# Kernel optimization log

Measured on AMD Instinct MI355X. Metric: run time of the kernel, lower is better.

The kernel has to match this reference:

```python
import jax, jax.numpy as jnp
import numpy as np

B, INS, OUTS, REF, H, NH, DH, NL, DFF = 8, 32, 64, 8, 256, 8, 32, 6, 1024
N = OUTS * OUTS  # 4096 tokens


def _ln(x, g, b, eps=1e-5):
    m = x.mean(-1, keepdims=True)
    v = ((x - m) ** 2).mean(-1, keepdims=True)
    return (x - m) * jax.lax.rsqrt(v + eps) * g + b


def _resize_ac(x, out):
    Hin = x.shape[1]
    c = jnp.arange(out) * ((Hin - 1) / (out - 1))
    i0 = jnp.floor(c).astype(jnp.int32)
    i1 = jnp.minimum(i0 + 1, Hin - 1)
    w = (c - i0).astype(x.dtype)
    x = x[:, i0] * (1 - w)[None, :, None, None] + x[:, i1] * w[None, :, None, None]
    x = x[:, :, i0] * (1 - w)[None, None, :, None] + x[:, :, i1] * w[None, None, :, None]
    return x


def _pos_embedding():
    # unified_pos_embedding: distance from each 64x64 grid point to each 8x8 ref point -> [N, REF^2]
    g = jnp.linspace(0.0, 1.0, OUTS)
    gx, gy = jnp.meshgrid(g, g, indexing='ij')
    grid = jnp.stack([gx, gy], -1).reshape(N, 2)
    r = jnp.linspace(0.0, 1.0, REF)
    rx, ry = jnp.meshgrid(r, r, indexing='ij')
    rgrid = jnp.stack([rx, ry], -1).reshape(REF * REF, 2)
    return jnp.sqrt(((grid[:, None, :] - rgrid[None, :, :]) ** 2).sum(-1))


def setup_inputs() -> dict:
    key = jax.random.key(0)
    ks = iter(jax.random.split(key, 64))
    def nrm(shape, std=0.02):
        return jax.random.normal(next(ks), shape, jnp.float32) * std
    inp = {'x': jax.random.normal(next(ks), (B, INS, INS, 3), jnp.float32)}
    inp['pre_W1'] = nrm((1 + REF * REF, 2 * H)); inp['pre_b1'] = jnp.zeros((2 * H,))
    inp['pre_W2'] = nrm((2 * H, H)); inp['pre_b2'] = jnp.zeros((H,))
    inp['placeholder'] = jax.random.uniform(next(ks), (H,), jnp.float32) / H
    inp['ln1_g'] = jnp.ones((NL, H)); inp['ln1_b'] = jnp.zeros((NL, H))
    inp['ln1a_g'] = jnp.ones((NL, H)); inp['ln1a_b'] = jnp.zeros((NL, H))
    inp['Wq'] = nrm((NL, H, H)); inp['Wk'] = nrm((NL, H, H)); inp['Wv'] = nrm((NL, H, H))
    inp['Wo'] = nrm((NL, H, H)); inp['bo'] = jnp.zeros((NL, H))
    inp['kn_g'] = jnp.ones((NL, NH, DH)); inp['kn_b'] = jnp.zeros((NL, NH, DH))
    inp['vn_g'] = jnp.ones((NL, NH, DH)); inp['vn_b'] = jnp.zeros((NL, NH, DH))
    inp['ln2_g'] = jnp.ones((NL, H)); inp['ln2_b'] = jnp.zeros((NL, H))
    inp['mlp_W1'] = nrm((NL, H, DFF)); inp['mlp_b1'] = jnp.zeros((NL, DFF))
    inp['mlp_W2'] = nrm((NL, DFF, H)); inp['mlp_b2'] = jnp.zeros((NL, H))
    inp['ln3_g'] = jnp.ones((H,)); inp['ln3_b'] = jnp.zeros((H,))
    inp['out_W'] = nrm((H, 1)); inp['out_b'] = jnp.zeros((1,))
    return inp


def reference(x, pre_W1, pre_b1, pre_W2, pre_b2, placeholder,
              ln1_g, ln1_b, ln1a_g, ln1a_b, Wq, Wk, Wv, Wo, bo,
              kn_g, kn_b, vn_g, vn_b, ln2_g, ln2_b,
              mlp_W1, mlp_b1, mlp_W2, mlp_b2, ln3_g, ln3_b, out_W, out_b):
    Bsz = x.shape[0]
    xr = _resize_ac(x, OUTS)[..., 2:3]          # [B,64,64,1]
    fx = xr.reshape(Bsz, N, 1)
    pos = _pos_embedding()                       # [N,64]
    fx = jnp.concatenate([fx, jnp.broadcast_to(pos[None], (Bsz, N, REF * REF))], -1)
    h = jax.nn.gelu(fx @ pre_W1 + pre_b1, approximate=False) @ pre_W2 + pre_b2
    h = h + placeholder
    for i in range(NL):
        xq = _ln(h, ln1_g[i], ln1_b[i])
        xkv = _ln(h, ln1a_g[i], ln1a_b[i])
        q = (xq @ Wq[i]).reshape(Bsz, N, NH, DH).transpose(0, 2, 1, 3)
        k = (xkv @ Wk[i]).reshape(Bsz, N, NH, DH).transpose(0, 2, 1, 3)
        v = (xkv @ Wv[i]).reshape(Bsz, N, NH, DH).transpose(0, 2, 1, 3)
        # galerkin attention: layernorm K and V over head dim (per-head affine), no softmax
        k = _ln(k, kn_g[i][:, None, :], kn_b[i][:, None, :])
        v = _ln(v, vn_g[i][:, None, :], vn_b[i][:, None, :])
        ctx = jnp.einsum('bhnd,bhne->bhde', k, v) / N   # [B,h,d,d]
        att = jnp.einsum('bhnd,bhde->bhne', q, ctx)
        att = att.transpose(0, 2, 1, 3).reshape(Bsz, N, H) @ Wo[i] + bo[i]
        h = h + att
        y = _ln(h, ln2_g[i], ln2_b[i])
        h = h + (jax.nn.gelu(y @ mlp_W1[i] + mlp_b1[i], approximate=False) @ mlp_W2[i] + mlp_b2[i])
    out = _ln(h, ln3_g, ln3_b) @ out_W + out_b
    return out.reshape(Bsz, OUTS, OUTS, 1)
```

## Files before the change

kernel.cpp:

```cpp
#include <hip/hip_runtime.h>
#include <cmath>

#define B_    8
#define INS_  32
#define OUTS_ 64
#define REF_  8
#define H_    256
#define NH_   8
#define DH_   32
#define NL_   6
#define DFF_  1024
#define N_    4096
#define M_    (B_*N_)
#define BUF   8388608ull

typedef unsigned short u16;
typedef unsigned int   u32;
typedef __attribute__((ext_vector_type(8))) short  bf16x8;
typedef __attribute__((ext_vector_type(4))) float  f32x4;
typedef __attribute__((ext_vector_type(4))) unsigned short u16x4;

struct bfpair { u16 hi, lo; };

__device__ __forceinline__ float gelu_f(float x){
    return 0.5f * x * (1.0f + erff(x * 0.70710678118654752f));
}
__device__ __forceinline__ u16 f2b(float f){
    union { float f; u32 u; } v; v.f = f;
    u32 r = v.u + 0x7fffu + ((v.u >> 16) & 1u);
    return (u16)(r >> 16);
}
__device__ __forceinline__ float b2f(u16 b){
    union { u32 u; float f; } v; v.u = ((u32)b) << 16;
    return v.f;
}
__device__ __forceinline__ bfpair fsplit(float x){
    bfpair p;
    p.hi = f2b(x);
    p.lo = f2b(x - b2f(p.hi));
    return p;
}

__global__ __launch_bounds__(256) void tconv_kernel(const float* __restrict__ in,
                                                    u16* __restrict__ oh,
                                                    u16* __restrict__ ol,
                                                    int K, int N, int Kpad, int nl,
                                                    int lstride)
{
    int idx = blockIdx.x * 256 + threadIdx.x;
    int per = N * Kpad;
    if (idx >= nl * per) return;
    int l = idx / per;
    int rem = idx - l * per;
    int n = rem / Kpad;
    int k = rem - n * Kpad;
    float v = (k < K) ? in[(size_t)l * K * N + (size_t)k * N + n] : 0.0f;
    bfpair p = fsplit(v);
    size_t o = (size_t)l * lstride + (size_t)n * Kpad + k;
    oh[o] = p.hi; ol[o] = p.lo;
}

__global__ __launch_bounds__(256) void lnfold_kernel(const float* __restrict__ kg,
                                                     const float* __restrict__ kb,
                                                     const float* __restrict__ vg,
                                                     const float* __restrict__ vb,
                                                     float* __restrict__ lng,
                                                     float* __restrict__ lnb)
{
    int idx = blockIdx.x * 256 + threadIdx.x;
    if (idx >= NL_ * 512) return;
    int l = idx >> 9, c = idx & 511;
    if (c < 256) { lng[idx] = kg[l * 256 + c];       lnb[idx] = kb[l * 256 + c]; }
    else         { lng[idx] = vg[l * 256 + c - 256]; lnb[idx] = vb[l * 256 + c - 256]; }
}

__global__ __launch_bounds__(256) void fx_kernel(const float* __restrict__ x,
                                                 u16* __restrict__ fh,
                                                 u16* __restrict__ fl)
{
    int idx = blockIdx.x * 256 + threadIdx.x;
    const int total = M_ * 96;
    if (idx >= total) return;
    int f   = idx % 96;
    int row = idx / 96;
    int n   = row % N_;
    int b   = row / N_;
    int gi = n >> 6, gj = n & 63;
    float v = 0.0f;
    if (f == 0) {
        float ci = gi * (31.0f / 63.0f);
        float cj = gj * (31.0f / 63.0f);
        int i0 = (int)floorf(ci); int i1 = min(i0 + 1, 31);
        int j0 = (int)floorf(cj); int j1 = min(j0 + 1, 31);
        float wi = ci - (float)i0, wj = cj - (float)j0;
        const float* xb = x + (size_t)b * INS_ * INS_ * 3 + 2;
        float v00 = xb[(i0 * 32 + j0) * 3];
        float v01 = xb[(i0 * 32 + j1) * 3];
        float v10 = xb[(i1 * 32 + j0) * 3];
        float v11 = xb[(i1 * 32 + j1) * 3];
        float r0 = v00 * (1.0f - wi) + v10 * wi;
        float r1 = v01 * (1.0f - wi) + v11 * wi;
        v = r0 * (1.0f - wj) + r1 * wj;
    } else if (f < 65) {
        int r = f - 1;
        int ri = r >> 3, rj = r & 7;
        float dx = gi * (1.0f / 63.0f) - ri * (1.0f / 7.0f);
        float dy = gj * (1.0f / 63.0f) - rj * (1.0f / 7.0f);
        v = sqrtf(dx * dx + dy * dy);
    }
    bfpair p = fsplit(v);
    fh[idx] = p.hi; fl[idx] = p.lo;
}

template<int EPI, int BN, int TERMS>
__global__ __launch_bounds__(256) void gemm_split(const u16* __restrict__ Ah,
                                                  const u16* __restrict__ Al,
                                                  const u16* __restrict__ Bh,
                                                  const u16* __restrict__ Bl,
                                                  float* __restrict__ Cf,
                                                  u16* __restrict__ Ch,
                                                  u16* __restrict__ Cl,
                                                  const float* __restrict__ bias,
                                                  const float* __restrict__ bias2,
                                                  const float* __restrict__ lng,
                                                  const float* __restrict__ lnb,
                                                  int M, int Nn, int K, int bstride)
{
    constexpr int NREP = BN / 32;
    constexpr int BROUNDS = BN / 64;
    __shared__ u16 AsH[4096];
    __shared__ u16 BsH[BN * 32];
    __shared__ u16 AsL[TERMS >= 2 ? 4096 : 1];
    __shared__ u16 BsL[TERMS == 3 ? BN * 32 : 1];
    const int tid = threadIdx.x;
    const int nwgx = gridDim.x;
    const int nwg  = nwgx * gridDim.y;
    const int bid  = blockIdx.y * nwgx + blockIdx.x;
    const int swz  = (bid & 7) * (nwg >> 3) + (bid >> 3);
    const int bm = (swz / nwgx) * 128;
    const int bn = (swz % nwgx) * BN;
    const u16* BhB = Bh + (size_t)(bm >> 12) * bstride;
    const u16* BlB = Bl + (size_t)(bm >> 12) * bstride;
    const int l  = tid & 63;
    const int w  = tid >> 6;
    const int wr = w >> 1, wc = w & 1;
    const int lrow = l & 15;
    const int kh   = l >> 4;

    f32x4 acc[4][NREP];
    #pragma unroll
    for (int m = 0; m < 4; ++m)
        #pragma unroll
        for (int n = 0; n < NREP; ++n)
            acc[m][n] = (f32x4){0.0f, 0.0f, 0.0f, 0.0f};

    for (int k0 = 0; k0 < K; k0 += 32) {
        #pragma unroll
        for (int i = 0; i < 2; ++i) {
            int L = i * 256 + tid;
            int row = L >> 2, ch = L & 3;
            size_t goffA = (size_t)(bm + row) * K + k0 + ch * 8;
            __builtin_amdgcn_global_load_lds(
                (const __attribute__((address_space(1))) void*)(Ah + goffA),
                (__attribute__((address_space(3))) void*)(AsH + L * 8), 16, 0, 0);
            if constexpr (TERMS >= 2)
                __builtin_amdgcn_global_load_lds(
                    (const __attribute__((address_space(1))) void*)(Al + goffA),
                    (__attribute__((address_space(3))) void*)(AsL + L * 8), 16, 0, 0);
        }
        #pragma unroll
        for (int i = 0; i < BROUNDS; ++i) {
            int L = i * 256 + tid;
            int row = L >> 2, ch = L & 3;
            size_t goffB = (size_t)(bn + row) * K + k0 + ch * 8;
            __builtin_amdgcn_global_load_lds(
                (const __attribute__((address_space(1))) void*)(BhB + goffB),
                (__attribute__((address_space(3))) void*)(BsH + L * 8), 16, 0, 0);
            if constexpr (TERMS == 3)
                __builtin_amdgcn_global_load_lds(
                    (const __attribute__((address_space(1))) void*)(BlB + goffB),
                    (__attribute__((address_space(3))) void*)(BsL + L * 8), 16, 0, 0);
        }
        __syncthreads();
        bf16x8 afh[4], afl[4], bfh[NREP], bfl[NREP];
        #pragma unroll
        for (int m = 0; m < 4; ++m) {
            int off = (wr * 64 + m * 16 + lrow) * 32 + kh * 8;
            afh[m] = *(const bf16x8*)(AsH + off);
            if constexpr (TERMS >= 2) afl[m] = *(const bf16x8*)(AsL + off);
        }
        #pragma unroll
        for (int n = 0; n < NREP; ++n) {
            int off = (wc * (BN / 2) + n * 16 + lrow) * 32 + kh * 8;
            bfh[n] = *(const bf16x8*)(BsH + off);
            if constexpr (TERMS == 3) bfl[n] = *(const bf16x8*)(BsL + off);
        }
        #pragma unroll
        for (int m = 0; m < 4; ++m)
            #pragma unroll
            for (int n = 0; n < NREP; ++n) {
                acc[m][n] = __builtin_amdgcn_mfma_f32_16x16x32_bf16(afh[m], bfh[n], acc[m][n], 0, 0, 0);
                if constexpr (TERMS >= 2)
                    acc[m][n] = __builtin_amdgcn_mfma_f32_16x16x32_bf16(afl[m], bfh[n], acc[m][n], 0, 0, 0);
                if constexpr (TERMS == 3)
                    acc[m][n] = __builtin_amdgcn_mfma_f32_16x16x32_bf16(afh[m], bfl[n], acc[m][n], 0, 0, 0);
            }
        __syncthreads();
    }

    const int row0 = bm + wr * 64;
    const int col0 = bn + wc * (BN / 2);

    if constexpr (EPI == 4) {
        #pragma unroll
        for (int m = 0; m < 4; ++m) {
            #pragma unroll
            for (int j = 0; j < 4; ++j) {
                int r = row0 + m * 16 + kh * 4 + j;
                #pragma unroll
                for (int hp = 0; hp < NREP / 2; ++hp) {
                    float a0 = acc[m][2 * hp + 0][j];
                    float a1 = acc[m][2 * hp + 1][j];
                    float s = a0 + a1;
                    s += __shfl_xor(s, 1); s += __shfl_xor(s, 2);
                    s += __shfl_xor(s, 4); s += __shfl_xor(s, 8);
                    float mean = s * (1.0f / 32.0f);
                    float d0 = a0 - mean, d1 = a1 - mean;
                    float q = d0 * d0 + d1 * d1;
                    q += __shfl_xor(q, 1); q += __shfl_xor(q, 2);
                    q += __shfl_xor(q, 4); q += __shfl_xor(q, 8);
                    float rstd = rsqrtf(q * (1.0f / 32.0f) + 1e-5f);
                    #pragma unroll
                    for (int t = 0; t < 2; ++t) {
                        int n = 2 * hp + t;
                        int col = col0 + n * 16 + lrow;
                        float dd = t ? d1 : d0;
                        float o = dd * rstd * lng[col] + lnb[col];
                        bfpair p = fsplit(o);
                        size_t idx = (size_t)r * Nn + col;
                        Ch[idx] = p.hi; Cl[idx] = p.lo;
                    }
                }
            }
        }
        return;
    }

    #pragma unroll
    for (int m = 0; m < 4; ++m) {
        #pragma unroll
        for (int n = 0; n < NREP; ++n) {
            int col = col0 + n * 16 + lrow;
            float bv = bias ? bias[col] : 0.0f;
            if (EPI == 3) bv += bias2[col];
            #pragma unroll
            for (int j = 0; j < 4; ++j) {
                int r = row0 + m * 16 + kh * 4 + j;
                float v = acc[m][n][j] + bv;
                size_t idx = (size_t)r * Nn + col;
                if (EPI == 0) {
                    bfpair p = fsplit(v);
                    Ch[idx] = p.hi; Cl[idx] = p.lo;
                } else if (EPI == 1) {
                    bfpair p = fsplit(gelu_f(v));
                    Ch[idx] = p.hi; Cl[idx] = p.lo;
                } else if (EPI == 2) {
                    Cf[idx] += v;
                } else {
                    Cf[idx] = v;
                }
            }
        }
    }
}

__global__ __launch_bounds__(256) void ln_dual_kernel(const float* __restrict__ h,
                                                      u16* __restrict__ o1h,
                                                      u16* __restrict__ o1l,
                                                      u16* __restrict__ o2h,
                                                      u16* __restrict__ o2l,
                                                      const float* __restrict__ g1,
                                                      const float* __restrict__ b1,
                                                      const float* __restrict__ g2,
                                                      const float* __restrict__ b2)
{
    int row  = blockIdx.x * 4 + (threadIdx.x >> 6);
    int lane = threadIdx.x & 63;
    const float4 v = ((const float4*)(h + (size_t)row * H_))[lane];
    float s = v.x + v.y + v.z + v.w;
    #pragma unroll
    for (int m = 1; m < 64; m <<= 1) s += __shfl_xor(s, m, 64);
    float mean = s * (1.0f / H_);
    float dx = v.x - mean, dy = v.y - mean, dz = v.z - mean, dw = v.w - mean;
    float sq = dx * dx + dy * dy + dz * dz + dw * dw;
    #pragma unroll
    for (int m = 1; m < 64; m <<= 1) sq += __shfl_xor(sq, m, 64);
    float rstd = rsqrtf(sq * (1.0f / H_) + 1e-5f);

    float4 G = ((const float4*)g1)[lane];
    float4 Bv = ((const float4*)b1)[lane];
    u16x4 oh, ol;
    bfpair p0 = fsplit(dx * rstd * G.x + Bv.x);
    bfpair p1 = fsplit(dy * rstd * G.y + Bv.y);
    bfpair p2 = fsplit(dz * rstd * G.z + Bv.z);
    bfpair p3 = fsplit(dw * rstd * G.w + Bv.w);
    oh.x = p0.hi; ol.x = p0.lo;
    oh.y = p1.hi; ol.y = p1.lo;
    oh.z = p2.hi; ol.z = p2.lo;
    oh.w = p3.hi; ol.w = p3.lo;
    ((u16x4*)(o1h + (size_t)row * H_))[lane] = oh;
    ((u16x4*)(o1l + (size_t)row * H_))[lane] = ol;
    if (o2h) {
        G = ((const float4*)g2)[lane];
        Bv = ((const float4*)b2)[lane];
        p0 = fsplit(dx * rstd * G.x + Bv.x);
        p1 = fsplit(dy * rstd * G.y + Bv.y);
        p2 = fsplit(dz * rstd * G.z + Bv.z);
        p3 = fsplit(dw * rstd * G.w + Bv.w);
        oh.x = p0.hi; ol.x = p0.lo;
        oh.y = p1.hi; ol.y = p1.lo;
        oh.z = p2.hi; ol.z = p2.lo;
        oh.w = p3.hi; ol.w = p3.lo;
        ((u16x4*)(o2h + (size_t)row * H_))[lane] = oh;
        ((u16x4*)(o2l + (size_t)row * H_))[lane] = ol;
    }
}

__global__ __launch_bounds__(256) void ctx_partial_kernel(const u16* __restrict__ kvh,
                                                          const u16* __restrict__ kvl,
                                                          float* __restrict__ ctxp)
{
    int bh = blockIdx.x;
    int split = blockIdx.y;
    int b = bh >> 3, hd = bh & 7;
    __shared__ float kc[8][32], vc[8][32];
    int tid = threadIdx.x;
    int rd = tid >> 5, dd = tid & 31;
    int d  = tid >> 3;
    int e0 = (tid & 7) * 4;
    float a0 = 0, a1 = 0, a2 = 0, a3 = 0;
    int nbase = split * 512;
    for (int it = 0; it < 64; ++it) {
        size_t off = ((size_t)(b * N_ + nbase + it * 8 + rd)) * 512 + hd * 32 + dd;
        kc[rd][dd] = b2f(kvh[off]) + b2f(kvl[off]);
        vc[rd][dd] = b2f(kvh[off + 256]) + b2f(kvl[off + 256]);
        __syncthreads();
        #pragma unroll
        for (int r = 0; r < 8; ++r) {
            float kd = kc[r][d];
            a0 += kd * vc[r][e0 + 0];
            a1 += kd * vc[r][e0 + 1];
            a2 += kd * vc[r][e0 + 2];
            a3 += kd * vc[r][e0 + 3];
        }
        __syncthreads();
    }
    float* out = ctxp + ((size_t)(split * 64 + bh)) * 1024 + d * 32 + e0;
    out[0] = a0; out[1] = a1; out[2] = a2; out[3] = a3;
}

__global__ __launch_bounds__(256) void compose1_kernel(const float* __restrict__ ctxp,
                                                       const float* __restrict__ Wo,
                                                       float* __restrict__ G)
{
    int b  = blockIdx.x >> 3;
    int hd = blockIdx.x & 7;
    __shared__ float cl[32][32];
    __shared__ float wl[32][256];
    int tid = threadIdx.x;
    {
        const float* src = ctxp + ((size_t)(b * 8 + hd)) * 1024;
        #pragma unroll
        for (int i = 0; i < 4; ++i) {
            float s = 0.0f;
            #pragma unroll
            for (int sp = 0; sp < 8; ++sp)
                s += src[(size_t)sp * 65536 + tid + 256 * i];
            ((float*)cl)[tid + 256 * i] = s * (1.0f / N_);
        }
        #pragma unroll
        for (int i = 0; i < 32; ++i)
            wl[i][tid] = Wo[(size_t)(hd * 32 + i) * 256 + tid];
    }
    __syncthreads();
    int j = tid;
    for (int d = 0; d < 32; ++d) {
        float s = 0.0f;
        #pragma unroll
        for (int e = 0; e < 32; ++e) s += cl[d][e] * wl[e][j];
        G[((size_t)b * 256 + hd * 32 + d) * 256 + j] = s;
    }
}

__global__ __launch_bounds__(256) void compose2_kernel(const float* __restrict__ Wq,
                                                       const float* __restrict__ G,
                                                       u16* __restrict__ fh,
                                                       u16* __restrict__ fl)
{
    int b  = blockIdx.x;
    int jg = blockIdx.y;
    __shared__ float Gs[16][256];
    int tid = threadIdx.x;
    #pragma unroll
    for (int jj = 0; jj < 16; ++jj)
        Gs[jj][tid] = G[(size_t)b * 65536 + (size_t)tid * 256 + jg * 16 + jj];
    __syncthreads();
    int i = tid;
    float acc[16];
    #pragma unroll
    for (int jj = 0; jj < 16; ++jj) acc[jj] = 0.0f;
    for (int m = 0; m < 256; ++m) {
        float wv = Wq[(size_t)i * 256 + m];
        #pragma unroll
        for (int jj = 0; jj < 16; ++jj) acc[jj] += wv * Gs[jj][m];
    }
    #pragma unroll
    for (int jj = 0; jj < 16; ++jj) {
        bfpair p = fsplit(acc[jj]);
        size_t off = (size_t)b * 65536 + (size_t)(jg * 16 + jj) * 256 + i;
        fh[off] = p.hi; fl[off] = p.lo;
    }
}

__global__ __launch_bounds__(256) void final_kernel(const float* __restrict__ h,
                                                    const float* __restrict__ g,
                                                    const float* __restrict__ bb,
                                                    const float* __restrict__ W,
                                                    const float* __restrict__ ob,
                                                    float* __restrict__ out)
{
    int row  = blockIdx.x * 4 + (threadIdx.x >> 6);
    int lane = threadIdx.x & 63;
    const float4 v = ((const float4*)(h + (size_t)row * H_))[lane];
    float s = v.x + v.y + v.z + v.w;
    #pragma unroll
    for (int m = 1; m < 64; m <<= 1) s += __shfl_xor(s, m, 64);
    float mean = s * (1.0f / H_);
    float dx = v.x - mean, dy = v.y - mean, dz = v.z - mean, dw = v.w - mean;
    float sq = dx * dx + dy * dy + dz * dz + dw * dw;
    #pragma unroll
    for (int m = 1; m < 64; m <<= 1) sq += __shfl_xor(sq, m, 64);
    float rstd = rsqrtf(sq * (1.0f / H_) + 1e-5f);
    float4 G = ((const float4*)g)[lane];
    float4 Bv = ((const float4*)bb)[lane];
    float4 Wv = ((const float4*)W)[lane];
    float s2 = (dx * rstd * G.x + Bv.x) * Wv.x
             + (dy * rstd * G.y + Bv.y) * Wv.y
             + (dz * rstd * G.z + Bv.z) * Wv.z
             + (dw * rstd * G.w + Bv.w) * Wv.w;
    #pragma unroll
    for (int m = 1; m < 64; m <<= 1) s2 += __shfl_xor(s2, m, 64);
    if (lane == 0) out[row] = s2 + ob[0];
}

extern "C" void kernel_launch(void* const* d_in, const int* in_sizes, int n_in,
                              void* d_out, int out_size, void* d_ws, size_t ws_size,
                              hipStream_t stream)
{
    const float* x        = (const float*)d_in[0];
    const float* pre_W1   = (const float*)d_in[1];
    const float* pre_b1   = (const float*)d_in[2];
    const float* pre_W2   = (const float*)d_in[3];
    const float* pre_b2   = (const float*)d_in[4];
    const float* placeholder = (const float*)d_in[5];
    const float* ln1_g    = (const float*)d_in[6];
    const float* ln1_b    = (const float*)d_in[7];
    const float* ln1a_g   = (const float*)d_in[8];
    const float* ln1a_b   = (const float*)d_in[9];
    const float* Wq       = (const float*)d_in[10];
    const float* Wk       = (const float*)d_in[11];
    const float* Wv       = (const float*)d_in[12];
    const float* Wo       = (const float*)d_in[13];
    const float* bo       = (const float*)d_in[14];
    const float* kn_g     = (const float*)d_in[15];
    const float* kn_b     = (const float*)d_in[16];
    const float* vn_g     = (const float*)d_in[17];
    const float* vn_b     = (const float*)d_in[18];
    const float* ln2_g    = (const float*)d_in[19];
    const float* ln2_b    = (const float*)d_in[20];
    const float* mlp_W1   = (const float*)d_in[21];
    const float* mlp_b1   = (const float*)d_in[22];
    const float* mlp_W2   = (const float*)d_in[23];
    const float* mlp_b2   = (const float*)d_in[24];
    const float* ln3_g    = (const float*)d_in[25];
    const float* ln3_b    = (const float*)d_in[26];
    const float* out_W    = (const float*)d_in[27];
    const float* out_b    = (const float*)d_in[28];

    float* ws   = (float*)d_ws;
    float* h    = ws;
    float* ctxp = ws + BUF;
    float* Gbuf = ctxp + 524288;
    float* lng  = Gbuf + 524288;
    float* lnb  = lng + NL_ * 512;
    u16* ub = (u16*)(lnb + NL_ * 512);
    u16* xa_h = ub;
    u16* xa_l = xa_h + BUF;
    u16* xb_h = xa_l + BUF;
    u16* xb_l = xb_h + BUF;
    u16* kv_h = xb_l + BUF;
    u16* kv_l = kv_h + 2 * BUF;
    u16* wt   = kv_l + 2 * BUF;
    u16* w_pre1h = wt;               u16* w_pre1l = w_pre1h + 49152;
    u16* w_pre2h = w_pre1l + 49152;  u16* w_pre2l = w_pre2h + 131072;
    u16* w_kvh = w_pre2l + 131072;   u16* w_kvl = w_kvh + 786432;
    u16* w_m1h = w_kvl + 786432;     u16* w_m1l = w_m1h + 1572864;
    u16* w_m2h = w_m1l + 1572864;    u16* w_m2l = w_m2h + 1572864;
    u16* f_h   = w_m2l + 1572864;    u16* f_l   = f_h + 524288;

    tconv_kernel<<<(512 * 96 + 255) / 256, 256, 0, stream>>>(pre_W1, w_pre1h, w_pre1l, 65, 512, 96, 1, 49152);
    tconv_kernel<<<(256 * 512 + 255) / 256, 256, 0, stream>>>(pre_W2, w_pre2h, w_pre2l, 512, 256, 512, 1, 131072);
    tconv_kernel<<<(6 * 65536 + 255) / 256, 256, 0, stream>>>(Wk, w_kvh, w_kvl, 256, 256, 256, 6, 131072);
    tconv_kernel<<<(6 * 65536 + 255) / 256, 256, 0, stream>>>(Wv, w_kvh + 65536, w_kvl + 65536, 256, 256, 256, 6, 131072);
    tconv_kernel<<<(6 * 262144 + 255) / 256, 256, 0, stream>>>(mlp_W1, w_m1h, w_m1l, 256, 1024, 256, 6, 262144);
    tconv_kernel<<<(6 * 262144 + 255) / 256, 256, 0, stream>>>(mlp_W2, w_m2h, w_m2l, 1024, 256, 1024, 6, 262144);
    lnfold_kernel<<<(NL_ * 512 + 255) / 256, 256, 0, stream>>>(kn_g, kn_b, vn_g, vn_b, lng, lnb);

    fx_kernel<<<(M_ * 96 + 255) / 256, 256, 0, stream>>>(x, xa_h, xa_l);
    for (int half = 0; half < 2; ++half) {
        size_t ao = (size_t)half * (M_ / 2) * 96;
        gemm_split<1, 128, 3><<<dim3(512 / 128, (M_ / 2) / 128), 256, 0, stream>>>(
            xa_h + ao, xa_l + ao, w_pre1h, w_pre1l, nullptr, xb_h, xb_l,
            pre_b1, nullptr, nullptr, nullptr, M_ / 2, 512, 96, 0);
        gemm_split<3, 128, 3><<<dim3(256 / 128, (M_ / 2) / 128), 256, 0, stream>>>(
            xb_h, xb_l, w_pre2h, w_pre2l, h + (size_t)half * (M_ / 2) * H_,
            nullptr, nullptr, pre_b2, placeholder, nullptr, nullptr, M_ / 2, 256, 512, 0);
    }

    for (int l = 0; l < NL_; ++l) {
        ln_dual_kernel<<<M_ / 4, 256, 0, stream>>>(
            h, xa_h, xa_l, xb_h, xb_l, ln1_g + l * H_, ln1_b + l * H_,
            ln1a_g + l * H_, ln1a_b + l * H_);

        gemm_split<4, 128, 2><<<dim3(512 / 128, M_ / 128), 256, 0, stream>>>(
            xb_h, xb_l, w_kvh + (size_t)l * 131072, w_kvl + (size_t)l * 131072,
            nullptr, kv_h, kv_l, nullptr, nullptr,
            lng + l * 512, lnb + l * 512, M_, 512, H_, 0);

        ctx_partial_kernel<<<dim3(64, 8), 256, 0, stream>>>(kv_h, kv_l, ctxp);
        compose1_kernel<<<64, 256, 0, stream>>>(ctxp, Wo + (size_t)l * 65536, Gbuf);
        compose2_kernel<<<dim3(8, 16), 256, 0, stream>>>(Wq + (size_t)l * 65536, Gbuf, f_h, f_l);

        gemm_split<2, 64, 2><<<dim3(256 / 64, M_ / 128), 256, 0, stream>>>(
            xa_h, xa_l, f_h, f_l, h, nullptr, nullptr, bo + l * H_, nullptr,
            nullptr, nullptr, M_, H_, H_, 65536);

        ln_dual_kernel<<<M_ / 4, 256, 0, stream>>>(
            h, xa_h, xa_l, nullptr, nullptr, ln2_g + l * H_, ln2_b + l * H_, nullptr, nullptr);

        for (int half = 0; half < 2; ++half) {
            size_t ao = (size_t)half * (M_ / 2) * H_;
            gemm_split<1, 128, 3><<<dim3(DFF_ / 128, (M_ / 2) / 128), 256, 0, stream>>>(
                xa_h + ao, xa_l + ao, w_m1h + (size_t)l * 262144, w_m1l + (size_t)l * 262144,
                nullptr, xb_h, kv_h, mlp_b1 + (size_t)l * DFF_, nullptr,
                nullptr, nullptr, M_ / 2, DFF_, H_, 0);
            gemm_split<2, 64, 3><<<dim3(256 / 64, (M_ / 2) / 128), 256, 0, stream>>>(
                xb_h, kv_h, w_m2h + (size_t)l * 262144, w_m2l + (size_t)l * 262144,
                h + ao, nullptr, nullptr, mlp_b2 + (size_t)l * H_, nullptr,
                nullptr, nullptr, M_ / 2, H_, DFF_, 0);
        }
    }

    final_kernel<<<M_ / 4, 256, 0, stream>>>(
        h, ln3_g, ln3_b, out_W, out_b, (float*)d_out);
}
```

Before: 2.179 ms.

## Double-buffer LDS tiles in split GEMM and merge pre-MLP halves

The split-bf16 GEMM now uses two LDS buffers per operand and issues the global-to-LDS loads for the next K tile before computing on the current one, so load latency can overlap the MFMA work. The pre-embedding MLP no longer runs in two halves; both GEMMs cover all rows in one launch each, with the larger kv buffers holding the 512-wide intermediate. This doubles LDS use per block, which can lower occupancy, especially for the 3-term variant. The loop still syncs only once per iteration, so correctness depends on the next-stage loads not being visible to the MFMA reads before the barrier.

```diff
diff --git a/kernel.cpp b/kernel.cpp
--- a/kernel.cpp
+++ b/kernel.cpp
@@ -128,10 +128,10 @@
 {
     constexpr int NREP = BN / 32;
     constexpr int BROUNDS = BN / 64;
-    __shared__ u16 AsH[4096];
-    __shared__ u16 BsH[BN * 32];
-    __shared__ u16 AsL[TERMS >= 2 ? 4096 : 1];
-    __shared__ u16 BsL[TERMS == 3 ? BN * 32 : 1];
+    __shared__ u16 AsH[2][4096];
+    __shared__ u16 BsH[2][BN * 32];
+    __shared__ u16 AsL[TERMS >= 2 ? 2 : 1][TERMS >= 2 ? 4096 : 1];
+    __shared__ u16 BsL[TERMS == 3 ? 2 : 1][TERMS == 3 ? BN * 32 : 1];
     const int tid = threadIdx.x;
     const int nwgx = gridDim.x;
     const int nwg  = nwgx * gridDim.y;
@@ -147,14 +147,7 @@
     const int lrow = l & 15;
     const int kh   = l >> 4;
 
-    f32x4 acc[4][NREP];
-    #pragma unroll
-    for (int m = 0; m < 4; ++m)
-        #pragma unroll
-        for (int n = 0; n < NREP; ++n)
-            acc[m][n] = (f32x4){0.0f, 0.0f, 0.0f, 0.0f};
-
-    for (int k0 = 0; k0 < K; k0 += 32) {
+    auto stage = [&](int k0, int s) {
         #pragma unroll
         for (int i = 0; i < 2; ++i) {
             int L = i * 256 + tid;
@@ -162,11 +155,11 @@
             size_t goffA = (size_t)(bm + row) * K + k0 + ch * 8;
             __builtin_amdgcn_global_load_lds(
                 (const __attribute__((address_space(1))) void*)(Ah + goffA),
-                (__attribute__((address_space(3))) void*)(AsH + L * 8), 16, 0, 0);
+                (__attribute__((address_space(3))) void*)(&AsH[s][L * 8]), 16, 0, 0);
             if constexpr (TERMS >= 2)
                 __builtin_amdgcn_global_load_lds(
                     (const __attribute__((address_space(1))) void*)(Al + goffA),
-                    (__attribute__((address_space(3))) void*)(AsL + L * 8), 16, 0, 0);
+                    (__attribute__((address_space(3))) void*)(&AsL[s][L * 8]), 16, 0, 0);
         }
         #pragma unroll
         for (int i = 0; i < BROUNDS; ++i) {
@@ -175,25 +168,39 @@
             size_t goffB = (size_t)(bn + row) * K + k0 + ch * 8;
             __builtin_amdgcn_global_load_lds(
                 (const __attribute__((address_space(1))) void*)(BhB + goffB),
-                (__attribute__((address_space(3))) void*)(BsH + L * 8), 16, 0, 0);
+                (__attribute__((address_space(3))) void*)(&BsH[s][L * 8]), 16, 0, 0);
             if constexpr (TERMS == 3)
                 __builtin_amdgcn_global_load_lds(
                     (const __attribute__((address_space(1))) void*)(BlB + goffB),
-                    (__attribute__((address_space(3))) void*)(BsL + L * 8), 16, 0, 0);
-        }
-        __syncthreads();
+                    (__attribute__((address_space(3))) void*)(&BsL[s][L * 8]), 16, 0, 0);
+        }
+    };
+
+    f32x4 acc[4][NREP];
+    #pragma unroll
+    for (int m = 0; m < 4; ++m)
+        #pragma unroll
+        for (int n = 0; n < NREP; ++n)
+            acc[m][n] = (f32x4){0.0f, 0.0f, 0.0f, 0.0f};
+
+    const int nk = K >> 5;
+    stage(0, 0);
+    __syncthreads();
+    int cur = 0;
+    for (int t = 0; t < nk; ++t) {
+        if (t + 1 < nk) stage((t + 1) << 5, cur ^ 1);
         bf16x8 afh[4], afl[4], bfh[NREP], bfl[NREP];
         #pragma unroll
         for (int m = 0; m < 4; ++m) {
             int off = (wr * 64 + m * 16 + lrow) * 32 + kh * 8;
-            afh[m] = *(const bf16x8*)(AsH + off);
-            if constexpr (TERMS >= 2) afl[m] = *(const bf16x8*)(AsL + off);
+            afh[m] = *(const bf16x8*)(&AsH[cur][off]);
+            if constexpr (TERMS >= 2) afl[m] = *(const bf16x8*)(&AsL[cur][off]);
         }
         #pragma unroll
         for (int n = 0; n < NREP; ++n) {
             int off = (wc * (BN / 2) + n * 16 + lrow) * 32 + kh * 8;
-            bfh[n] = *(const bf16x8*)(BsH + off);
-            if constexpr (TERMS == 3) bfl[n] = *(const bf16x8*)(BsL + off);
+            bfh[n] = *(const bf16x8*)(&BsH[cur][off]);
+            if constexpr (TERMS == 3) bfl[n] = *(const bf16x8*)(&BsL[cur][off]);
         }
         #pragma unroll
         for (int m = 0; m < 4; ++m)
@@ -206,6 +213,7 @@
                     acc[m][n] = __builtin_amdgcn_mfma_f32_16x16x32_bf16(afh[m], bfl[n], acc[m][n], 0, 0, 0);
             }
         __syncthreads();
+        cur ^= 1;
     }
 
     const int row0 = bm + wr * 64;
@@ -517,15 +525,12 @@
     lnfold_kernel<<<(NL_ * 512 + 255) / 256, 256, 0, stream>>>(kn_g, kn_b, vn_g, vn_b, lng, lnb);
 
     fx_kernel<<<(M_ * 96 + 255) / 256, 256, 0, stream>>>(x, xa_h, xa_l);
-    for (int half = 0; half < 2; ++half) {
-        size_t ao = (size_t)half * (M_ / 2) * 96;
-        gemm_split<1, 128, 3><<<dim3(512 / 128, (M_ / 2) / 128), 256, 0, stream>>>(
-            xa_h + ao, xa_l + ao, w_pre1h, w_pre1l, nullptr, xb_h, xb_l,
-            pre_b1, nullptr, nullptr, nullptr, M_ / 2, 512, 96, 0);
-        gemm_split<3, 128, 3><<<dim3(256 / 128, (M_ / 2) / 128), 256, 0, stream>>>(
-            xb_h, xb_l, w_pre2h, w_pre2l, h + (size_t)half * (M_ / 2) * H_,
-            nullptr, nullptr, pre_b2, placeholder, nullptr, nullptr, M_ / 2, 256, 512, 0);
-    }
+    gemm_split<1, 128, 3><<<dim3(512 / 128, M_ / 128), 256, 0, stream>>>(
+        xa_h, xa_l, w_pre1h, w_pre1l, nullptr, kv_h, kv_l,
+        pre_b1, nullptr, nullptr, nullptr, M_, 512, 96, 0);
+    gemm_split<3, 128, 3><<<dim3(256 / 128, M_ / 128), 256, 0, stream>>>(
+        kv_h, kv_l, w_pre2h, w_pre2l, h, nullptr, nullptr,
+        pre_b2, placeholder, nullptr, nullptr, M_, 256, 512, 0);
 
     for (int l = 0; l < NL_; ++l) {
         ln_dual_kernel<<<M_ / 4, 256, 0, stream>>>(
```

New measurement: 2.131 ms. 1.02x faster.
